# Performance work log

Measured on AMD Instinct MI355X. Metric: run time of the kernel, lower is better.

The kernel has to match this reference:

```python
import jax, jax.numpy as jnp
import numpy as np
import math

N_HEADS = 16

def setup_inputs() -> dict:
    key = jax.random.key(0)
    qkv = jax.random.normal(key, (2, 2048, 3072), dtype=jnp.float32)
    return {"qkv": qkv}

def reference(qkv):
    bs, n_ctx, width = qkv.shape
    attn_ch = width // N_HEADS // 3
    scale = 1.0 / math.sqrt(math.sqrt(attn_ch))
    qkv = qkv.reshape(bs, n_ctx, N_HEADS, 3 * attn_ch)
    q, k, v = jnp.split(qkv, 3, axis=-1)  # each [b, s, h, c]
    # scores: [b, h, t, s]
    weight = jnp.einsum('bthc,bshc->bhts', q * scale, k * scale)
    weight = jax.nn.softmax(weight.astype(jnp.float32), axis=-1).astype(qkv.dtype)
    out = jnp.einsum('bhts,bshc->bthc', weight, v)
    return out.reshape(bs, n_ctx, -1)
```

## Files before the change

kernel.cpp:

```cpp
#include <hip/hip_runtime.h>

typedef __attribute__((ext_vector_type(4))) float f32x4;
typedef __attribute__((ext_vector_type(8))) short s16x8;
typedef __attribute__((ext_vector_type(4))) unsigned short u16x4;

#define NH 16
#define SEQ 2048
#define WIDTH 3072
#define DH 64
#define KVB 64
#define NT (SEQ / KVB)
#define QSCALE 0.125f
#define SHIFT 8.0f

__device__ __forceinline__ unsigned short f2bf(float f) {
  union { __bf16 b; unsigned short u; } cv;
  cv.b = (__bf16)f;
  return cv.u;
}

__global__ __launch_bounds__(256, 2) void attn_fwd(const float* __restrict__ qkv,
                                                   float* __restrict__ out) {
  int bid0 = (int)blockIdx.x;
  int bid = (bid0 & 7) * 64 + (bid0 >> 3);
  const int qb = bid & 15;
  const int h  = (bid >> 4) & 15;
  const int b  = bid >> 8;

  const int tid  = (int)threadIdx.x;
  const int lane = tid & 63;
  const int wid  = tid >> 6;
  const int col  = lane & 15;
  const int hi   = lane >> 4;
  const int cx   = (col & 7) << 3;

  __shared__ __align__(16) unsigned short sK[2][KVB * 64];
  __shared__ __align__(16) unsigned short sV[2][DH * 64];

  const size_t base = (size_t)b * SEQ * WIDTH + (size_t)h * (3 * DH);
  const int q0 = qb * 128 + wid * 32;

  s16x8 qf[2][2];
#pragma unroll
  for (int rb = 0; rb < 2; ++rb) {
    const float* qp = qkv + base + (size_t)(q0 + rb * 16 + col) * WIDTH;
#pragma unroll
    for (int c = 0; c < 2; ++c) {
      const f32x4 f0 = *(const f32x4*)(qp + 32 * c + 8 * hi);
      const f32x4 f1 = *(const f32x4*)(qp + 32 * c + 8 * hi + 4);
      s16x8 v;
#pragma unroll
      for (int j = 0; j < 4; ++j) {
        v[j]     = (short)f2bf(f0[j] * QSCALE);
        v[4 + j] = (short)f2bf(f1[j] * QSCALE);
      }
      qf[rb][c] = v;
    }
  }

  f32x4 oacc[2][4];
  float l_[2] = {0.0f, 0.0f};
#pragma unroll
  for (int rb = 0; rb < 2; ++rb)
#pragma unroll
    for (int nc = 0; nc < 4; ++nc)
#pragma unroll
      for (int r = 0; r < 4; ++r) oacc[rb][nc][r] = 0.0f;

  const int krow = tid >> 2, kdc = (tid & 3) * 16;
  const int vrg = tid & 15, vdg = tid >> 4;
  const int pbase = 32 * (vrg >> 3) + 8 * (vrg & 3) + 4 * ((vrg >> 2) & 1);

  f32x4 kr[4], vr[4];

  auto load_tile = [&](int t) {
    const float* kg = qkv + base + (size_t)(t * KVB + krow) * WIDTH + DH + kdc;
#pragma unroll
    for (int i = 0; i < 4; ++i) kr[i] = *(const f32x4*)(kg + 4 * i);
    const float* vg = qkv + base + (size_t)(t * KVB + vrg * 4) * WIDTH + 2 * DH + vdg * 4;
#pragma unroll
    for (int rr = 0; rr < 4; ++rr) vr[rr] = *(const f32x4*)(vg + (size_t)rr * WIDTH);
  };

  auto write_tile = [&](int pb) {
#pragma unroll
    for (int i = 0; i < 2; ++i) {
      s16x8 w;
#pragma unroll
      for (int j = 0; j < 4; ++j) {
        w[j]     = (short)f2bf(kr[2 * i][j]);
        w[4 + j] = (short)f2bf(kr[2 * i + 1][j]);
      }
      const int e = (krow * 64 + kdc + 8 * i) ^ ((krow & 7) << 3);
      *(s16x8*)&sK[pb][e] = w;
    }
#pragma unroll
    for (int dd = 0; dd < 4; ++dd) {
      const int d = vdg * 4 + dd;
      u16x4 w;
#pragma unroll
      for (int rr = 0; rr < 4; ++rr) w[rr] = f2bf(vr[rr][dd]);
      const int e = (d * 64 + pbase) ^ ((d & 7) << 3);
      *(u16x4*)&sV[pb][e] = w;
    }
  };

  load_tile(0);
  write_tile(0);

  for (int t = 0; t < NT; ++t) {
    const int pb = t & 1;
    __syncthreads();
    if (t + 1 < NT) load_tile(t + 1);

    s16x8 kf[4][2];
#pragma unroll
    for (int g = 0; g < 4; ++g)
#pragma unroll
      for (int c = 0; c < 2; ++c)
        kf[g][c] = *(const s16x8*)&sK[pb][((16 * g + col) * 64 + 32 * c + 8 * hi) ^ cx];

    s16x8 vf[2][4];
#pragma unroll
    for (int u = 0; u < 2; ++u)
#pragma unroll
      for (int nc = 0; nc < 4; ++nc)
        vf[u][nc] = *(const s16x8*)&sV[pb][((16 * nc + col) * 64 + 32 * u + 8 * hi) ^ cx];

#pragma unroll
    for (int rb = 0; rb < 2; ++rb) {
      f32x4 sa[4];
#pragma unroll
      for (int g = 0; g < 4; ++g)
#pragma unroll
        for (int r = 0; r < 4; ++r) sa[g][r] = -SHIFT;
      __builtin_amdgcn_s_setprio(1);
#pragma unroll
      for (int g = 0; g < 4; ++g)
#pragma unroll
        for (int c = 0; c < 2; ++c)
          sa[g] = __builtin_amdgcn_mfma_f32_16x16x32_bf16(kf[g][c], qf[rb][c], sa[g], 0, 0, 0);
      __builtin_amdgcn_s_setprio(0);

      float pr[16];
#pragma unroll
      for (int g = 0; g < 4; ++g)
#pragma unroll
        for (int r = 0; r < 4; ++r) pr[g * 4 + r] = __expf(sa[g][r]);
      const float t0 = (pr[0] + pr[1]) + (pr[2] + pr[3]);
      const float t1 = (pr[4] + pr[5]) + (pr[6] + pr[7]);
      const float t2 = (pr[8] + pr[9]) + (pr[10] + pr[11]);
      const float t3 = (pr[12] + pr[13]) + (pr[14] + pr[15]);
      l_[rb] += (t0 + t1) + (t2 + t3);

      s16x8 pa[2];
#pragma unroll
      for (int u = 0; u < 2; ++u) {
        s16x8 w;
#pragma unroll
        for (int j = 0; j < 8; ++j) w[j] = (short)f2bf(pr[8 * u + j]);
        pa[u] = w;
      }
      __builtin_amdgcn_s_setprio(1);
#pragma unroll
      for (int u = 0; u < 2; ++u)
#pragma unroll
        for (int nc = 0; nc < 4; ++nc)
          oacc[rb][nc] = __builtin_amdgcn_mfma_f32_16x16x32_bf16(pa[u], vf[u][nc], oacc[rb][nc], 0, 0, 0);
      __builtin_amdgcn_s_setprio(0);
    }

    if (t + 1 < NT) write_tile((t + 1) & 1);
  }

#pragma unroll
  for (int rb = 0; rb < 2; ++rb) {
    float lv = l_[rb];
    lv += __shfl_xor(lv, 16);
    lv += __shfl_xor(lv, 32);
#pragma unroll
    for (int r = 0; r < 4; ++r) {
      const float lt = __shfl(lv, 4 * hi + r);
      const float inv = 1.0f / lt;
      const int q = q0 + rb * 16 + 4 * hi + r;
      float* op = out + ((size_t)b * SEQ + q) * (NH * DH) + h * DH;
#pragma unroll
      for (int nc = 0; nc < 4; ++nc)
        op[nc * 16 + col] = oacc[rb][nc][r] * inv;
    }
  }
}

extern "C" void kernel_launch(void* const* d_in, const int* in_sizes, int n_in,
                              void* d_out, int out_size, void* d_ws, size_t ws_size,
                              hipStream_t stream) {
  const float* qkv = (const float*)d_in[0];
  float* out = (float*)d_out;
  (void)in_sizes; (void)n_in; (void)out_size; (void)d_ws; (void)ws_size;
  attn_fwd<<<dim3(512), dim3(256), 0, stream>>>(qkv, out);
}
```

Before: 123.4 us.

## Halve query rows per block to double grid size and occupancy

Each block now handles 64 query rows instead of 128, with each wave owning a single 16-row block rather than two, so the grid doubles to 1024 blocks and launch bounds allow 4 blocks per CU. The aim is to fill all CUs of the MI355X and give more waves for latency hiding, at the cost of streaming and converting every K/V tile twice as often, halving K/V reuse per load. Per-tile LDS staging and bf16 conversion work per MFMA also doubles.

```diff
diff --git a/kernel.cpp b/kernel.cpp
--- a/kernel.cpp
+++ b/kernel.cpp
@@ -19,13 +19,13 @@
   return cv.u;
 }
 
-__global__ __launch_bounds__(256, 2) void attn_fwd(const float* __restrict__ qkv,
+__global__ __launch_bounds__(256, 4) void attn_fwd(const float* __restrict__ qkv,
                                                    float* __restrict__ out) {
   int bid0 = (int)blockIdx.x;
-  int bid = (bid0 & 7) * 64 + (bid0 >> 3);
-  const int qb = bid & 15;
-  const int h  = (bid >> 4) & 15;
-  const int b  = bid >> 8;
+  int bid = (bid0 & 7) * 128 + (bid0 >> 3);
+  const int qb = bid & 31;
+  const int h  = (bid >> 5) & 15;
+  const int b  = bid >> 9;
 
   const int tid  = (int)threadIdx.x;
   const int lane = tid & 63;
@@ -38,12 +38,11 @@
   __shared__ __align__(16) unsigned short sV[2][DH * 64];
 
   const size_t base = (size_t)b * SEQ * WIDTH + (size_t)h * (3 * DH);
-  const int q0 = qb * 128 + wid * 32;
+  const int q0 = qb * 64 + wid * 16;
 
-  s16x8 qf[2][2];
-#pragma unroll
-  for (int rb = 0; rb < 2; ++rb) {
-    const float* qp = qkv + base + (size_t)(q0 + rb * 16 + col) * WIDTH;
+  s16x8 qf[2];
+  {
+    const float* qp = qkv + base + (size_t)(q0 + col) * WIDTH;
 #pragma unroll
     for (int c = 0; c < 2; ++c) {
       const f32x4 f0 = *(const f32x4*)(qp + 32 * c + 8 * hi);
@@ -54,18 +53,16 @@
         v[j]     = (short)f2bf(f0[j] * QSCALE);
         v[4 + j] = (short)f2bf(f1[j] * QSCALE);
       }
-      qf[rb][c] = v;
+      qf[c] = v;
     }
   }
 
-  f32x4 oacc[2][4];
-  float l_[2] = {0.0f, 0.0f};
+  f32x4 oacc[4];
+  float l_ = 0.0f;
 #pragma unroll
-  for (int rb = 0; rb < 2; ++rb)
+  for (int nc = 0; nc < 4; ++nc)
 #pragma unroll
-    for (int nc = 0; nc < 4; ++nc)
-#pragma unroll
-      for (int r = 0; r < 4; ++r) oacc[rb][nc][r] = 0.0f;
+    for (int r = 0; r < 4; ++r) oacc[nc][r] = 0.0f;
 
   const int krow = tid >> 2, kdc = (tid & 3) * 16;
   const int vrg = tid & 15, vdg = tid >> 4;
@@ -127,66 +124,62 @@
       for (int nc = 0; nc < 4; ++nc)
         vf[u][nc] = *(const s16x8*)&sV[pb][((16 * nc + col) * 64 + 32 * u + 8 * hi) ^ cx];
 
+    f32x4 sa[4];
 #pragma unroll
-    for (int rb = 0; rb < 2; ++rb) {
-      f32x4 sa[4];
+    for (int g = 0; g < 4; ++g)
 #pragma unroll
-      for (int g = 0; g < 4; ++g)
+      for (int r = 0; r < 4; ++r) sa[g][r] = -SHIFT;
+    __builtin_amdgcn_s_setprio(1);
 #pragma unroll
-        for (int r = 0; r < 4; ++r) sa[g][r] = -SHIFT;
-      __builtin_amdgcn_s_setprio(1);
+    for (int g = 0; g < 4; ++g)
 #pragma unroll
-      for (int g = 0; g < 4; ++g)
+      for (int c = 0; c < 2; ++c)
+        sa[g] = __builtin_amdgcn_mfma_f32_16x16x32_bf16(kf[g][c], qf[c], sa[g], 0, 0, 0);
+    __builtin_amdgcn_s_setprio(0);
+
+    float pr[16];
 #pragma unroll
-        for (int c = 0; c < 2; ++c)
-          sa[g] = __builtin_amdgcn_mfma_f32_16x16x32_bf16(kf[g][c], qf[rb][c], sa[g], 0, 0, 0);
-      __builtin_amdgcn_s_setprio(0);
+    for (int g = 0; g < 4; ++g)
+#pragma unroll
+      for (int r = 0; r < 4; ++r) pr[g * 4 + r] = __expf(sa[g][r]);
+    const float t0 = (pr[0] + pr[1]) + (pr[2] + pr[3]);
+    const float t1 = (pr[4] + pr[5]) + (pr[6] + pr[7]);
+    const float t2 = (pr[8] + pr[9]) + (pr[10] + pr[11]);
+    const float t3 = (pr[12] + pr[13]) + (pr[14] + pr[15]);
+    l_ += (t0 + t1) + (t2 + t3);
 
-      float pr[16];
+    s16x8 pa[2];
 #pragma unroll
-      for (int g = 0; g < 4; ++g)
+    for (int u = 0; u < 2; ++u) {
+      s16x8 w;
 #pragma unroll
-        for (int r = 0; r < 4; ++r) pr[g * 4 + r] = __expf(sa[g][r]);
-      const float t0 = (pr[0] + pr[1]) + (pr[2] + pr[3]);
-      const float t1 = (pr[4] + pr[5]) + (pr[6] + pr[7]);
-      const float t2 = (pr[8] + pr[9]) + (pr[10] + pr[11]);
-      const float t3 = (pr[12] + pr[13]) + (pr[14] + pr[15]);
-      l_[rb] += (t0 + t1) + (t2 + t3);
-
-      s16x8 pa[2];
+      for (int j = 0; j < 8; ++j) w[j] = (short)f2bf(pr[8 * u + j]);
+      pa[u] = w;
+    }
+    __builtin_amdgcn_s_setprio(1);
 #pragma unroll
-      for (int u = 0; u < 2; ++u) {
-        s16x8 w;
+    for (int u = 0; u < 2; ++u)
 #pragma unroll
-        for (int j = 0; j < 8; ++j) w[j] = (short)f2bf(pr[8 * u + j]);
-        pa[u] = w;
-      }
-      __builtin_amdgcn_s_setprio(1);
-#pragma unroll
-      for (int u = 0; u < 2; ++u)
-#pragma unroll
-        for (int nc = 0; nc < 4; ++nc)
-          oacc[rb][nc] = __builtin_amdgcn_mfma_f32_16x16x32_bf16(pa[u], vf[u][nc], oacc[rb][nc], 0, 0, 0);
-      __builtin_amdgcn_s_setprio(0);
-    }
+      for (int nc = 0; nc < 4; ++nc)
+        oacc[nc] = __builtin_amdgcn_mfma_f32_16x16x32_bf16(pa[u], vf[u][nc], oacc[nc], 0, 0, 0);
+    __builtin_amdgcn_s_setprio(0);
 
     if (t + 1 < NT) write_tile((t + 1) & 1);
   }
 
-#pragma unroll
-  for (int rb = 0; rb < 2; ++rb) {
-    float lv = l_[rb];
+  {
+    float lv = l_;
     lv += __shfl_xor(lv, 16);
     lv += __shfl_xor(lv, 32);
 #pragma unroll
     for (int r = 0; r < 4; ++r) {
       const float lt = __shfl(lv, 4 * hi + r);
       const float inv = 1.0f / lt;
-      const int q = q0 + rb * 16 + 4 * hi + r;
+      const int q = q0 + 4 * hi + r;
       float* op = out + ((size_t)b * SEQ + q) * (NH * DH) + h * DH;
 #pragma unroll
       for (int nc = 0; nc < 4; ++nc)
-        op[nc * 16 + col] = oacc[rb][nc][r] * inv;
+        op[nc * 16 + col] = oacc[nc][r] * inv;
     }
   }
 }
@@ -197,5 +190,5 @@
   const float* qkv = (const float*)d_in[0];
   float* out = (float*)d_out;
   (void)in_sizes; (void)n_in; (void)out_size; (void)d_ws; (void)ws_size;
-  attn_fwd<<<dim3(512), dim3(256), 0, stream>>>(qkv, out);
+  attn_fwd<<<dim3(1024), dim3(256), 0, stream>>>(qkv, out);
 }
```

Measured after the change: 375.1 us. 3.04x slower.
